# Performance work log

Hardware: AMD Instinct MI355X
Metric: run time of the kernel (lower is better)

Reference implementation:

```python
import jax, jax.numpy as jnp
import numpy as np

N_HEADS = 16
D_MODEL = 1024
D_K = D_MODEL // N_HEADS


def setup_inputs() -> dict:
    key = jax.random.key(0)
    ks = jax.random.split(key, 7)
    B, S = 2, 2048
    init = 0.02
    return {
        "query": jax.random.normal(ks[0], (B, S, D_MODEL), dtype=jnp.float32),
        "key": jax.random.normal(ks[1], (B, S, D_MODEL), dtype=jnp.float32),
        "value": jax.random.normal(ks[2], (B, S, D_MODEL), dtype=jnp.float32),
        "W_q": jax.random.normal(ks[3], (D_MODEL, D_MODEL), dtype=jnp.float32) * init,
        "W_k": jax.random.normal(ks[4], (D_MODEL, D_MODEL), dtype=jnp.float32) * init,
        "W_v": jax.random.normal(ks[5], (D_MODEL, D_MODEL), dtype=jnp.float32) * init,
        "W_o": jax.random.normal(ks[6], (D_MODEL, D_MODEL), dtype=jnp.float32) * init,
    }


def _split_heads(x):
    # (B, S, d_model) -> (B, H, S, d_k)
    B, S, _ = x.shape
    return x.reshape(B, S, N_HEADS, D_K).transpose(0, 2, 1, 3)


def reference(query, key, value, W_q, W_k, W_v, W_o):
    scale = jnp.sqrt(jnp.asarray(D_K, dtype=query.dtype))
    # torch Linear: y = x @ W.T
    Q = _split_heads(query @ W_q.T)   # (B,H,Sq,dk)
    K = _split_heads(key @ W_k.T)     # (B,H,Sk,dk)
    V = _split_heads(value @ W_v.T)   # (B,H,Sk,dk)
    scores = jnp.einsum("bhqd,bhkd->bhqk", Q, K) / scale
    attn = jax.nn.softmax(scores, axis=-1)           # (B,H,Sq,Sk); dropout p=0 -> identity
    attn_weights = attn.mean(axis=1)                 # (B,Sq,Sk) interpretable weights
    head_out = jnp.einsum("bhqk,bhkd->bqhd", attn, V)  # (B,Sq,H,dk)
    # NOTE: the original computes a head-gating (W_h) whose result is overwritten
    # by the concat below -> dead code, omitted.
    B, Sq = head_out.shape[0], head_out.shape[1]
    out = head_out.reshape(B, Sq, D_MODEL) @ W_o.T   # (B,Sq,d_model)
    return (out, attn_weights)
```

## Files before the change

### kernel.cpp

```cpp
#include <hip/hip_runtime.h>
#include <hip/hip_bf16.h>

#define Bq 2
#define Hh 16
#define Ss 2048
#define Dm 1024
#define Dk 64
#define QSC 0.18033688f

typedef _Float16 f16x8 __attribute__((ext_vector_type(8)));
typedef _Float16 f16x4 __attribute__((ext_vector_type(4)));
typedef _Float16 f16x2 __attribute__((ext_vector_type(2)));
typedef float    f32x4 __attribute__((ext_vector_type(4)));


__device__ __forceinline__ void gl_lds16(const void* g, void* lds) {
    __builtin_amdgcn_global_load_lds(
        (const __attribute__((address_space(1))) void*)g,
        (__attribute__((address_space(3))) void*)lds, 16, 0, 0);
}

extern "C" __device__ float __ocml_exp2_f32(float);

__device__ __forceinline__ float exp2_fast(float x) {
#if __has_builtin(__builtin_amdgcn_exp2f)
    return __builtin_amdgcn_exp2f(x);
#else
    return __ocml_exp2_f32(x);
#endif
}

__device__ __forceinline__ float rcp_fast(float x) {
#if __has_builtin(__builtin_amdgcn_rcpf)
    return __builtin_amdgcn_rcpf(x);
#else
    float r; asm("v_rcp_f32 %0, %1" : "=v"(r) : "v"(x)); return r;
#endif
}

__device__ __forceinline__ f16x2 pk_f16(float a, float b) {
    return __builtin_bit_cast(f16x2, __builtin_amdgcn_cvt_pkrtz(a, b));
}

__global__ __launch_bounds__(256) void convert_kernel(
    const float* __restrict__ q, const float* __restrict__ k,
    const float* __restrict__ v, const float* __restrict__ wq,
    const float* __restrict__ wk, const float* __restrict__ wv,
    const float* __restrict__ wo,
    _Float16* __restrict__ qd, _Float16* __restrict__ kd,
    _Float16* __restrict__ vd, _Float16* __restrict__ wd)
{
    int seg = blockIdx.y;
    const float* src; _Float16* dst; int n4;
    switch (seg) {
        case 0: src = q; dst = qd; n4 = 1048576; break;
        case 1: src = k; dst = kd; n4 = 1048576; break;
        case 2: src = v; dst = vd; n4 = 1048576; break;
        default:
            src = (seg == 3) ? wq : (seg == 4) ? wk : (seg == 5) ? wv : wo;
            dst = wd + (size_t)(seg - 3) * 1048576;
            n4 = 262144;
    }
    for (int i = blockIdx.x * 256 + threadIdx.x; i < n4; i += gridDim.x * 256) {
        float4 x = ((const float4*)src)[i];
        f16x4 h = {(_Float16)x.x, (_Float16)x.y, (_Float16)x.z, (_Float16)x.w};
        ((f16x4*)dst)[i] = h;
    }
}

__global__ __launch_bounds__(256) void gemm_qkv(
    const _Float16* __restrict__ qf, const _Float16* __restrict__ kf,
    const _Float16* __restrict__ vf, const _Float16* __restrict__ Wh,
    _Float16* __restrict__ Qd, _Float16* __restrict__ Kd,
    _Float16* __restrict__ Vd)
{
    __shared__ _Float16 As[128 * 32];
    __shared__ _Float16 Ws[128 * 32];
    int z = blockIdx.z;
    const _Float16* A = (z == 0) ? qf : (z == 1) ? kf : vf;
    const _Float16* W = Wh + (size_t)z * (Dm * Dm);
    int t = threadIdx.x, lane = t & 63, w = t >> 6;
    int quad = lane >> 4, l15 = lane & 15;
    int wm = w & 1, wn = w >> 1;
    int n0 = blockIdx.x * 128, m0 = blockIdx.y * 128;

    f32x4 acc[4][4] = {};
    for (int k0 = 0; k0 < Dm; k0 += 32) {
        __syncthreads();
        for (int j = 0; j < 2; ++j) {
            int ca = w * 128 + j * 64 + lane;
            int row = ca >> 2, c8 = (ca & 3) * 8;
            gl_lds16(&A[(size_t)(m0 + row) * Dm + k0 + c8],
                     &As[(size_t)(w * 128 + j * 64) * 8]);
            gl_lds16(&W[(size_t)(n0 + row) * Dm + k0 + c8],
                     &Ws[(size_t)(w * 128 + j * 64) * 8]);
        }
        __syncthreads();
        f16x8 af[4], bf[4];
        for (int mi = 0; mi < 4; ++mi)
            af[mi] = *(const f16x8*)&As[(wm * 64 + mi * 16 + l15) * 32 + quad * 8];
        for (int ni = 0; ni < 4; ++ni)
            bf[ni] = *(const f16x8*)&Ws[(wn * 64 + ni * 16 + l15) * 32 + quad * 8];
        for (int mi = 0; mi < 4; ++mi)
            for (int ni = 0; ni < 4; ++ni)
                acc[mi][ni] = __builtin_amdgcn_mfma_f32_16x16x32_f16(
                    af[mi], bf[ni], acc[mi][ni], 0, 0, 0);
    }
    _Float16* Y = (z == 0) ? Qd : (z == 1) ? Kd : Vd;
    float osc = (z == 0) ? QSC : 1.0f;
    for (int mi = 0; mi < 4; ++mi)
        for (int ni = 0; ni < 4; ++ni)
            for (int r = 0; r < 4; ++r) {
                int m = m0 + wm * 64 + mi * 16 + quad * 4 + r;
                int n = n0 + wn * 64 + ni * 16 + l15;
                int b = m >> 11, s = m & (Ss - 1);
                int h = n >> 6,  d = n & 63;
                _Float16 v = (_Float16)(acc[mi][ni][r] * osc);
                if (z < 2)
                    Y[(((size_t)(b * Hh + h) * Ss + s) << 6) + d] = v;
                else
                    Y[((size_t)(b * Hh + h) * Dk + d) * Ss + s] = v;
            }
}

__global__ __launch_bounds__(256) void gemm_out(
    const _Float16* __restrict__ HO, const _Float16* __restrict__ Woh,
    float* __restrict__ out)
{
    __shared__ _Float16 As[128 * 32];
    __shared__ _Float16 Ws[64 * 32];
    int t = threadIdx.x, lane = t & 63, w = t >> 6;
    int quad = lane >> 4, l15 = lane & 15;
    int n0 = blockIdx.x * 64, m0 = blockIdx.y * 128;

    f32x4 acc[2][4] = {};
    for (int k0 = 0; k0 < Dm; k0 += 32) {
        __syncthreads();
        for (int j = 0; j < 2; ++j) {
            int ca = w * 128 + j * 64 + lane;
            int row = ca >> 2, c8 = (ca & 3) * 8;
            gl_lds16(&HO[(size_t)(m0 + row) * Dm + k0 + c8],
                     &As[(size_t)(w * 128 + j * 64) * 8]);
        }
        {
            int cw = w * 64 + lane;
            int row = cw >> 2, c8 = (cw & 3) * 8;
            gl_lds16(&Woh[(size_t)(n0 + row) * Dm + k0 + c8],
                     &Ws[(size_t)(w * 64) * 8]);
        }
        __syncthreads();
        f16x8 af[2], bf[4];
        for (int mi = 0; mi < 2; ++mi)
            af[mi] = *(const f16x8*)&As[(w * 32 + mi * 16 + l15) * 32 + quad * 8];
        for (int ni = 0; ni < 4; ++ni)
            bf[ni] = *(const f16x8*)&Ws[(ni * 16 + l15) * 32 + quad * 8];
        for (int mi = 0; mi < 2; ++mi)
            for (int ni = 0; ni < 4; ++ni)
                acc[mi][ni] = __builtin_amdgcn_mfma_f32_16x16x32_f16(
                    af[mi], bf[ni], acc[mi][ni], 0, 0, 0);
    }
    for (int mi = 0; mi < 2; ++mi)
        for (int ni = 0; ni < 4; ++ni)
            for (int r = 0; r < 4; ++r) {
                int m = m0 + w * 32 + mi * 16 + quad * 4 + r;
                int n = n0 + ni * 16 + l15;
                out[(size_t)m * Dm + n] = acc[mi][ni][r];
            }
}

__global__ __launch_bounds__(256) void flash_kernel(
    const _Float16* __restrict__ Qh, const _Float16* __restrict__ Kh,
    const _Float16* __restrict__ Vt, _Float16* __restrict__ Op,
    float* __restrict__ lp)
{
    __shared__ alignas(16) char Ks[8192];
    __shared__ alignas(16) char Vs[8192];
    __shared__ alignas(16) char Ps[4][4096];
    int t = threadIdx.x;
    int lane = t & 63, w = t >> 6;
    int quad = lane >> 4, l15 = lane & 15;
    int bh = blockIdx.x;
    int q0 = blockIdx.y * 128 + w * 32;
    int ks = blockIdx.z;
    int kt0 = ks * 16, kt1 = kt0 + 16;

    const _Float16* Qp = Qh + (size_t)bh * Ss * Dk;
    const _Float16* Kp = Kh + (size_t)bh * Ss * Dk;
    const _Float16* Vp = Vt + (size_t)bh * Dk * Ss;

    f16x8 qf[2][2];
#pragma unroll
    for (int qh = 0; qh < 2; ++qh)
#pragma unroll
        for (int kf = 0; kf < 2; ++kf)
            qf[qh][kf] = *(const f16x8*)
                &Qp[(size_t)(q0 + qh * 16 + l15) * Dk + kf * 32 + quad * 8];

    const _Float16 one = (_Float16)1.0f;
    const f16x8 ones = {one, one, one, one, one, one, one, one};

    int srow0 = t >> 3;
    int colh  = (t & 7) * 8;
    int sw0 = srow0 * 128 + ((colh * 2) ^ ((srow0 & 7) << 4));
    int sw1 = sw0 + 32 * 128;
    int swz = (l15 & 7) << 4;

    f16x8 kr0 = *(const f16x8*)&Kp[(size_t)(kt0 * 64 + srow0) * Dk + colh];
    f16x8 kr1 = *(const f16x8*)&Kp[(size_t)(kt0 * 64 + srow0 + 32) * Dk + colh];
    f16x8 vr0 = *(const f16x8*)&Vp[(size_t)srow0 * Ss + kt0 * 64 + colh];
    f16x8 vr1 = *(const f16x8*)&Vp[(size_t)(srow0 + 32) * Ss + kt0 * 64 + colh];

    f32x4 o_acc[2][4] = {};
    f32x4 l_acc[2] = {};
    char* Pw = Ps[w];

    for (int kt = kt0; kt < kt1; ++kt) {
        __syncthreads();
        *(f16x8*)(Ks + sw0) = kr0;
        *(f16x8*)(Ks + sw1) = kr1;
        *(f16x8*)(Vs + sw0) = vr0;
        *(f16x8*)(Vs + sw1) = vr1;
        if (kt + 1 < kt1) {
            kr0 = *(const f16x8*)&Kp[(size_t)((kt + 1) * 64 + srow0) * Dk + colh];
            kr1 = *(const f16x8*)&Kp[(size_t)((kt + 1) * 64 + srow0 + 32) * Dk + colh];
            vr0 = *(const f16x8*)&Vp[(size_t)srow0 * Ss + (kt + 1) * 64 + colh];
            vr1 = *(const f16x8*)&Vp[(size_t)(srow0 + 32) * Ss + (kt + 1) * 64 + colh];
        }
        __syncthreads();

#pragma unroll
        for (int nt = 0; nt < 4; ++nt) {
            const char* rb = Ks + ((nt * 16 + l15) << 7);
            f16x8 kf0 = *(const f16x8*)(rb + ((quad * 16) ^ swz));
            f16x8 kf1 = *(const f16x8*)(rb + ((64 + quad * 16) ^ swz));
#pragma unroll
            for (int qh = 0; qh < 2; ++qh) {
                f32x4 z = {};
                z = __builtin_amdgcn_mfma_f32_16x16x32_f16(kf0, qf[qh][0], z, 0, 0, 0);
                z = __builtin_amdgcn_mfma_f32_16x16x32_f16(kf1, qf[qh][1], z, 0, 0, 0);
                f16x2 h0 = pk_f16(exp2_fast(z[0]), exp2_fast(z[1]));
                f16x2 h1 = pk_f16(exp2_fast(z[2]), exp2_fast(z[3]));
                f16x4 hv = {h0[0], h0[1], h1[0], h1[1]};
                int prow = qh * 16 + l15;
                *(f16x4*)(Pw + prow * 128 +
                          (((nt * 32 + quad * 8)) ^ ((prow & 7) << 4))) = hv;
            }
        }

        f16x8 vf[4][2];
#pragma unroll
        for (int dt = 0; dt < 4; ++dt) {
            const char* rb = Vs + ((dt * 16 + l15) << 7);
            vf[dt][0] = *(const f16x8*)(rb + ((quad * 16) ^ swz));
            vf[dt][1] = *(const f16x8*)(rb + ((64 + quad * 16) ^ swz));
        }
#pragma unroll
        for (int qh = 0; qh < 2; ++qh) {
            const char* pr = Pw + ((qh * 16 + l15) << 7);
            f16x8 pf0 = *(const f16x8*)(pr + ((quad * 16) ^ swz));
            f16x8 pf1 = *(const f16x8*)(pr + ((64 + quad * 16) ^ swz));
            l_acc[qh] = __builtin_amdgcn_mfma_f32_16x16x32_f16(
                pf0, ones, l_acc[qh], 0, 0, 0);
            l_acc[qh] = __builtin_amdgcn_mfma_f32_16x16x32_f16(
                pf1, ones, l_acc[qh], 0, 0, 0);
#pragma unroll
            for (int dt = 0; dt < 4; ++dt) {
                o_acc[qh][dt] = __builtin_amdgcn_mfma_f32_16x16x32_f16(
                    pf0, vf[dt][0], o_acc[qh][dt], 0, 0, 0);
                o_acc[qh][dt] = __builtin_amdgcn_mfma_f32_16x16x32_f16(
                    pf1, vf[dt][1], o_acc[qh][dt], 0, 0, 0);
            }
        }
    }

    _Float16* Od = Op + (size_t)ks * (Bq * Hh * Ss * Dk) + (size_t)bh * Ss * Dk;
#pragma unroll
    for (int qh = 0; qh < 2; ++qh) {
#pragma unroll
        for (int dt = 0; dt < 4; ++dt)
#pragma unroll
            for (int r = 0; r < 4; ++r) {
                int q = q0 + qh * 16 + quad * 4 + r;
                Od[(size_t)q * Dk + dt * 16 + l15] = (_Float16)o_acc[qh][dt][r];
            }
        if (l15 == 0)
#pragma unroll
            for (int r = 0; r < 4; ++r)
                lp[(size_t)ks * 65536 + (size_t)bh * Ss + q0 + qh * 16 +
                   quad * 4 + r] = l_acc[qh][r];
    }
}

__global__ __launch_bounds__(256) void reduce_kernel(
    const _Float16* __restrict__ Op, const float* __restrict__ lp,
    _Float16* __restrict__ HO, float* __restrict__ lw)
{
    int i = blockIdx.x * 256 + threadIdx.x;
    int d4  = i & 15;
    int row = i >> 4;
    f16x4 a = ((const f16x4*)Op)[i];
    f16x4 b = ((const f16x4*)Op)[i + 1048576];
    float l = lp[row] + lp[65536 + row];
    float inv = rcp_fast(l);
    int bh = row >> 11, q = row & (Ss - 1);
    int b_ = bh >> 4,  h = bh & 15;
    f16x4 o;
    for (int j = 0; j < 4; ++j)
        o[j] = (_Float16)(((float)a[j] + (float)b[j]) * inv);
    *(f16x4*)&HO[((size_t)(b_ * Ss + q)) * Dm + h * Dk + d4 * 4] = o;
    if (d4 == 0) lw[row] = l;
}

__global__ __launch_bounds__(256) void attn_mean_kernel(
    const _Float16* __restrict__ Qh, const _Float16* __restrict__ Kh,
    const float* __restrict__ lw, float* __restrict__ out_attn)
{
    __shared__ alignas(16) char Ks[8192];
    int t = threadIdx.x;
    int lane = t & 63, w = t >> 6;
    int quad = lane >> 4, l15 = lane & 15;
    int k0 = blockIdx.x * 64;
    int q0 = blockIdx.y * 128;
    int b  = blockIdx.z;
    int qrow = q0 + w * 32;

    int srow0 = t >> 3;
    int colh  = (t & 7) * 8;
    int sw0 = srow0 * 128 + ((colh * 2) ^ ((srow0 & 7) << 4));
    int sw1 = sw0 + 32 * 128;
    int swz = (l15 & 7) << 4;

    f16x8 kr0, kr1, qn[2][2];
    float4 ln[2];
    {
        size_t base = (size_t)(b * Hh) * Ss;
        kr0 = *(const f16x8*)&Kh[(base + k0 + srow0) * Dk + colh];
        kr1 = *(const f16x8*)&Kh[(base + k0 + srow0 + 32) * Dk + colh];
#pragma unroll
        for (int qh = 0; qh < 2; ++qh) {
            qn[qh][0] = *(const f16x8*)&Qh[(base + qrow + qh * 16 + l15) * Dk + quad * 8];
            qn[qh][1] = *(const f16x8*)&Qh[(base + qrow + qh * 16 + l15) * Dk + 32 + quad * 8];
            ln[qh] = *(const float4*)&lw[base + qrow + qh * 16 + quad * 4];
        }
    }

    f32x4 acc[2][4] = {};
    for (int h = 0; h < Hh; ++h) {
        __syncthreads();
        *(f16x8*)(Ks + sw0) = kr0;
        *(f16x8*)(Ks + sw1) = kr1;
        f16x8 qf[2][2];
        float4 lv[2];
#pragma unroll
        for (int qh = 0; qh < 2; ++qh) {
            qf[qh][0] = qn[qh][0]; qf[qh][1] = qn[qh][1]; lv[qh] = ln[qh];
        }
        if (h < Hh - 1) {
            size_t base = (size_t)(b * Hh + h + 1) * Ss;
            kr0 = *(const f16x8*)&Kh[(base + k0 + srow0) * Dk + colh];
            kr1 = *(const f16x8*)&Kh[(base + k0 + srow0 + 32) * Dk + colh];
#pragma unroll
            for (int qh = 0; qh < 2; ++qh) {
                qn[qh][0] = *(const f16x8*)&Qh[(base + qrow + qh * 16 + l15) * Dk + quad * 8];
                qn[qh][1] = *(const f16x8*)&Qh[(base + qrow + qh * 16 + l15) * Dk + 32 + quad * 8];
                ln[qh] = *(const float4*)&lw[base + qrow + qh * 16 + quad * 4];
            }
        }
        __syncthreads();

        float ir[2][4];
#pragma unroll
        for (int qh = 0; qh < 2; ++qh) {
            ir[qh][0] = rcp_fast(lv[qh].x); ir[qh][1] = rcp_fast(lv[qh].y);
            ir[qh][2] = rcp_fast(lv[qh].z); ir[qh][3] = rcp_fast(lv[qh].w);
        }
#pragma unroll
        for (int nt = 0; nt < 4; ++nt) {
            const char* rb = Ks + ((nt * 16 + l15) << 7);
            f16x8 b0 = *(const f16x8*)(rb + ((quad * 16) ^ swz));
            f16x8 b1 = *(const f16x8*)(rb + ((64 + quad * 16) ^ swz));
#pragma unroll
            for (int qh = 0; qh < 2; ++qh) {
                f32x4 z = {};
                z = __builtin_amdgcn_mfma_f32_16x16x32_f16(qf[qh][0], b0, z, 0, 0, 0);
                z = __builtin_amdgcn_mfma_f32_16x16x32_f16(qf[qh][1], b1, z, 0, 0, 0);
#pragma unroll
                for (int r = 0; r < 4; ++r)
                    acc[qh][nt][r] += exp2_fast(z[r]) * ir[qh][r];
            }
        }
    }

#pragma unroll
    for (int qh = 0; qh < 2; ++qh)
#pragma unroll
        for (int nt = 0; nt < 4; ++nt)
#pragma unroll
            for (int r = 0; r < 4; ++r) {
                int q = qrow + qh * 16 + quad * 4 + r;
                out_attn[((size_t)(b * Ss + q)) * Ss + k0 + nt * 16 + l15] =
                    acc[qh][nt][r] * (1.0f / Hh);
            }
}

extern "C" void kernel_launch(void* const* d_in, const int* in_sizes, int n_in,
                              void* d_out, int out_size, void* d_ws, size_t ws_size,
                              hipStream_t stream) {
    const float* query = (const float*)d_in[0];
    const float* key   = (const float*)d_in[1];
    const float* value = (const float*)d_in[2];
    const float* Wq    = (const float*)d_in[3];
    const float* Wk    = (const float*)d_in[4];
    const float* Wv    = (const float*)d_in[5];
    const float* Wo    = (const float*)d_in[6];

    float* out      = (float*)d_out;
    float* attn_out = out + (size_t)4194304;

    _Float16* HO  = (_Float16*)attn_out;
    _Float16* qf  = (_Float16*)(attn_out + 2097152);
    _Float16* kf  = qf + 4194304;
    _Float16* vf  = kf + 4194304;
    _Float16* Op  = qf;
    float*    lp  = (float*)(Op + 2 * 4194304);

    _Float16* Qh = (_Float16*)d_ws;
    _Float16* Kh = Qh + (size_t)4194304;
    _Float16* Vt = Kh + (size_t)4194304;
    _Float16* Wh = Vt + (size_t)4194304;
    float*    lw = (float*)(Wh + (size_t)4194304);

    convert_kernel<<<dim3(256, 7), 256, 0, stream>>>(
        query, key, value, Wq, Wk, Wv, Wo, qf, kf, vf, Wh);

    gemm_qkv<<<dim3(8, 32, 3), 256, 0, stream>>>(qf, kf, vf, Wh, Qh, Kh, Vt);

    flash_kernel<<<dim3(Bq * Hh, Ss / 128, 2), 256, 0, stream>>>(Qh, Kh, Vt, Op, lp);

    reduce_kernel<<<4096, 256, 0, stream>>>(Op, lp, HO, lw);

    gemm_out<<<dim3(16, 32), 256, 0, stream>>>(HO, Wh + (size_t)3 * 1048576, out);

    attn_mean_kernel<<<dim3(Ss / 64, Ss / 128, Bq), 256, 0, stream>>>(
        Qh, Kh, lw, attn_out);
}
```

Baseline: 277.6 us.

## Fuse split-K reduce into output GEMM and coalesce V-transpose stores via LDS

The separate reduce_kernel is removed. gemm_out now loads both flash-attention partial outputs and their row sums, normalizes them in registers, writes the result to LDS, and stores lw. This removes one launch and the HO intermediate round trip. The cost is that the A-tile loads become synchronous register loads instead of async global-to-LDS copies, and each of the 16 column blocks redoes the normalization. In gemm_qkv, the transposed V output is staged through a swizzled LDS buffer so it can be written with 16-byte coalesced stores instead of strided 2-byte scatters.

```diff
diff --git a/kernel.cpp b/kernel.cpp
--- a/kernel.cpp
+++ b/kernel.cpp
@@ -74,8 +74,9 @@
     _Float16* __restrict__ Qd, _Float16* __restrict__ Kd,
     _Float16* __restrict__ Vd)
 {
-    __shared__ _Float16 As[128 * 32];
-    __shared__ _Float16 Ws[128 * 32];
+    __shared__ alignas(16) char smem[32768];
+    _Float16* As = (_Float16*)smem;
+    _Float16* Ws = (_Float16*)(smem + 8192);
     int z = blockIdx.z;
     const _Float16* A = (z == 0) ? qf : (z == 1) ? kf : vf;
     const _Float16* W = Wh + (size_t)z * (Dm * Dm);
@@ -106,26 +107,48 @@
                 acc[mi][ni] = __builtin_amdgcn_mfma_f32_16x16x32_f16(
                     af[mi], bf[ni], acc[mi][ni], 0, 0, 0);
     }
-    _Float16* Y = (z == 0) ? Qd : (z == 1) ? Kd : Vd;
-    float osc = (z == 0) ? QSC : 1.0f;
-    for (int mi = 0; mi < 4; ++mi)
-        for (int ni = 0; ni < 4; ++ni)
-            for (int r = 0; r < 4; ++r) {
-                int m = m0 + wm * 64 + mi * 16 + quad * 4 + r;
-                int n = n0 + wn * 64 + ni * 16 + l15;
-                int b = m >> 11, s = m & (Ss - 1);
-                int h = n >> 6,  d = n & 63;
-                _Float16 v = (_Float16)(acc[mi][ni][r] * osc);
-                if (z < 2)
-                    Y[(((size_t)(b * Hh + h) * Ss + s) << 6) + d] = v;
-                else
-                    Y[((size_t)(b * Hh + h) * Dk + d) * Ss + s] = v;
-            }
+
+    if (z == 2) {
+        __syncthreads();
+        for (int mi = 0; mi < 4; ++mi)
+            for (int ni = 0; ni < 4; ++ni) {
+                int n_l = wn * 64 + ni * 16 + l15;
+                int m_b = wm * 64 + mi * 16 + quad * 4;
+                f16x4 hv = {(_Float16)acc[mi][ni][0], (_Float16)acc[mi][ni][1],
+                            (_Float16)acc[mi][ni][2], (_Float16)acc[mi][ni][3]};
+                *(f16x4*)(smem + n_l * 256 + ((m_b * 2) ^ ((n_l & 7) << 4))) = hv;
+            }
+        __syncthreads();
+        int b = m0 >> 11, sb = m0 & (Ss - 1);
+        for (int p = 0; p < 8; ++p) {
+            int cid = p * 256 + t;
+            int rown = cid >> 4, c16 = cid & 15;
+            f16x8 v = *(const f16x8*)(smem + rown * 256 +
+                                      ((c16 * 16) ^ ((rown & 7) << 4)));
+            int n = n0 + rown;
+            int h = n >> 6, d = n & 63;
+            *(f16x8*)&Vd[(((size_t)(b * Hh + h) * Dk + d) << 11) + sb + c16 * 8] = v;
+        }
+    } else {
+        _Float16* Y = (z == 0) ? Qd : Kd;
+        float osc = (z == 0) ? QSC : 1.0f;
+        for (int mi = 0; mi < 4; ++mi)
+            for (int ni = 0; ni < 4; ++ni)
+                for (int r = 0; r < 4; ++r) {
+                    int m = m0 + wm * 64 + mi * 16 + quad * 4 + r;
+                    int n = n0 + wn * 64 + ni * 16 + l15;
+                    int b = m >> 11, s = m & (Ss - 1);
+                    int h = n >> 6,  d = n & 63;
+                    Y[(((size_t)(b * Hh + h) * Ss + s) << 6) + d] =
+                        (_Float16)(acc[mi][ni][r] * osc);
+                }
+    }
 }
 
 __global__ __launch_bounds__(256) void gemm_out(
-    const _Float16* __restrict__ HO, const _Float16* __restrict__ Woh,
-    float* __restrict__ out)
+    const _Float16* __restrict__ Op, const float* __restrict__ lp,
+    const _Float16* __restrict__ Woh, float* __restrict__ out,
+    float* __restrict__ lw)
 {
     __shared__ _Float16 As[128 * 32];
     __shared__ _Float16 Ws[64 * 32];
@@ -139,8 +162,22 @@
         for (int j = 0; j < 2; ++j) {
             int ca = w * 128 + j * 64 + lane;
             int row = ca >> 2, c8 = (ca & 3) * 8;
-            gl_lds16(&HO[(size_t)(m0 + row) * Dm + k0 + c8],
-                     &As[(size_t)(w * 128 + j * 64) * 8]);
+            int m = m0 + row;
+            int kk = k0 + c8;
+            int bh = ((m >> 11) << 4) + (kk >> 6);
+            int q = m & (Ss - 1);
+            int lidx = (bh << 11) + q;
+            size_t oidx = (((size_t)lidx) << 6) + (kk & 63);
+            f16x8 a  = *(const f16x8*)&Op[oidx];
+            f16x8 bv = *(const f16x8*)&Op[(size_t)4194304 + oidx];
+            float l = lp[lidx] + lp[65536 + lidx];
+            float inv = rcp_fast(l);
+            f16x8 hv;
+#pragma unroll
+            for (int e = 0; e < 8; ++e)
+                hv[e] = (_Float16)(((float)a[e] + (float)bv[e]) * inv);
+            *(f16x8*)&As[row * 32 + c8] = hv;
+            if ((kk & 63) == 0) lw[lidx] = l;
         }
         {
             int cw = w * 64 + lane;
@@ -291,26 +328,6 @@
     }
 }
 
-__global__ __launch_bounds__(256) void reduce_kernel(
-    const _Float16* __restrict__ Op, const float* __restrict__ lp,
-    _Float16* __restrict__ HO, float* __restrict__ lw)
-{
-    int i = blockIdx.x * 256 + threadIdx.x;
-    int d4  = i & 15;
-    int row = i >> 4;
-    f16x4 a = ((const f16x4*)Op)[i];
-    f16x4 b = ((const f16x4*)Op)[i + 1048576];
-    float l = lp[row] + lp[65536 + row];
-    float inv = rcp_fast(l);
-    int bh = row >> 11, q = row & (Ss - 1);
-    int b_ = bh >> 4,  h = bh & 15;
-    f16x4 o;
-    for (int j = 0; j < 4; ++j)
-        o[j] = (_Float16)(((float)a[j] + (float)b[j]) * inv);
-    *(f16x4*)&HO[((size_t)(b_ * Ss + q)) * Dm + h * Dk + d4 * 4] = o;
-    if (d4 == 0) lw[row] = l;
-}
-
 __global__ __launch_bounds__(256) void attn_mean_kernel(
     const _Float16* __restrict__ Qh, const _Float16* __restrict__ Kh,
     const float* __restrict__ lw, float* __restrict__ out_attn)
@@ -417,7 +434,6 @@
     float* out      = (float*)d_out;
     float* attn_out = out + (size_t)4194304;
 
-    _Float16* HO  = (_Float16*)attn_out;
     _Float16* qf  = (_Float16*)(attn_out + 2097152);
     _Float16* kf  = qf + 4194304;
     _Float16* vf  = kf + 4194304;
@@ -437,9 +453,8 @@
 
     flash_kernel<<<dim3(Bq * Hh, Ss / 128, 2), 256, 0, stream>>>(Qh, Kh, Vt, Op, lp);
 
-    reduce_kernel<<<4096, 256, 0, stream>>>(Op, lp, HO, lw);
-
-    gemm_out<<<dim3(16, 32), 256, 0, stream>>>(HO, Wh + (size_t)3 * 1048576, out);
+    gemm_out<<<dim3(16, 32), 256, 0, stream>>>(
+        Op, lp, Wh + (size_t)3 * 1048576, out, lw);
 
     attn_mean_kernel<<<dim3(Ss / 64, Ss / 128, Bq), 256, 0, stream>>>(
         Qh, Kh, lw, attn_out);
```

Measured after the change: 292.8 us. +5.5%, slower.
